# Performance work log

Measured on AMD Instinct MI355X. Metric: run time of the kernel, lower is better.

The kernel has to match this reference:

```python
import jax, jax.numpy as jnp
import numpy as np

N_ATOMS = 1_000_000
N_PAIRS = 32_000_000
N_MOL = 10_000

def setup_inputs() -> dict:
    key = jax.random.key(0)
    k1, k2, k3, k4, k5 = jax.random.split(key, 5)
    charges = jax.random.normal(k1, (N_ATOMS, 1), dtype=jnp.float32)
    # distances in [0.5, 2.5) to avoid divide-by-zero
    pair_dist = jax.random.uniform(k2, (N_PAIRS,), dtype=jnp.float32, minval=0.5, maxval=2.5)
    pair_first = jax.random.randint(k3, (N_PAIRS,), 0, N_ATOMS)
    pair_second = jax.random.randint(k4, (N_PAIRS,), 0, N_ATOMS)
    mol_index = jax.random.randint(k5, (N_ATOMS,), 0, N_MOL)
    return {
        "charges": charges,
        "pair_dist": pair_dist,
        "pair_first": pair_first,
        "pair_second": pair_second,
        "mol_index": mol_index,
        "n_molecules": N_MOL,
        "energy_conversion_factor": jnp.float32(14.399645),
    }

def reference(charges, pair_dist, pair_first, pair_second, mol_index, n_molecules, energy_conversion_factor):
    n_atoms = charges.shape[0]
    # gather charge of second atom in each pair, scale by 1/r  -> [n_pairs, 1]
    voltage_pairs = energy_conversion_factor * (charges[pair_second] / pair_dist[:, None])
    # scatter-add pair voltages onto first atom -> [n_atoms, 1]
    voltage_atom = jax.ops.segment_sum(voltage_pairs, pair_first, num_segments=n_atoms)
    # per-atom coulomb energy, then segment-sum over molecules
    coulomb_atom = voltage_atom * charges
    coulomb_molecules = 0.5 * jax.ops.segment_sum(coulomb_atom, mol_index, num_segments=n_molecules)
    return coulomb_molecules, voltage_atom
```

## Files before the change

kernel.cpp:

```cpp
#include <hip/hip_runtime.h>
#include <hip/hip_fp16.h>

#define BUCKET_BITS 12
#define BUCKET_SIZE 4096
#define NB 256
#define PPB 8192
#define BLK_A 256
#define MOL_BLOCKS 64


__global__ void init_cursors(int* __restrict__ cur, int nbuckets, int cap) {
    int b = blockIdx.x * blockDim.x + threadIdx.x;
    if (b < nbuckets) cur[b] = b * cap;
}

__global__ __launch_bounds__(BLK_A) void pair_scatter(
    const int4*   __restrict__ first4,
    const int4*   __restrict__ second4,
    const float4* __restrict__ dist4,
    const float*  __restrict__ charges,
    const float*  __restrict__ ecf_p,
    int* __restrict__ cur,
    unsigned* __restrict__ entries,
    int n_pairs4) {
    __shared__ unsigned stag[PPB];
    __shared__ int hist[NB];
    __shared__ int scanA[NB];
    __shared__ int lofs[NB + 1];
    __shared__ int gadj[NB];

    const int tid = threadIdx.x;
    hist[tid] = 0;
    __syncthreads();

    const int groups = PPB / 4;
    const int base4 = blockIdx.x * groups;

    #pragma unroll
    for (int it = 0; it < groups / BLK_A; ++it) {
        int g = base4 + it * BLK_A + tid;
        if (g < n_pairs4) {
            int4 f = first4[g];
            atomicAdd(&hist[f.x >> BUCKET_BITS], 1);
            atomicAdd(&hist[f.y >> BUCKET_BITS], 1);
            atomicAdd(&hist[f.z >> BUCKET_BITS], 1);
            atomicAdd(&hist[f.w >> BUCKET_BITS], 1);
        }
    }
    __syncthreads();

    scanA[tid] = hist[tid];
    __syncthreads();
    for (int off = 1; off < NB; off <<= 1) {
        int v = scanA[tid];
        if (tid >= off) v += scanA[tid - off];
        __syncthreads();
        scanA[tid] = v;
        __syncthreads();
    }
    if (tid == 0) lofs[0] = 0;
    lofs[tid + 1] = scanA[tid];
    __syncthreads();

    int cnt = hist[tid];
    if (cnt > 0) gadj[tid] = atomicAdd(&cur[tid], cnt) - lofs[tid];
    hist[tid] = lofs[tid];
    __syncthreads();

    const float ecf = *ecf_p;

    #pragma unroll
    for (int it = 0; it < groups / BLK_A; ++it) {
        int g = base4 + it * BLK_A + tid;
        if (g < n_pairs4) {
            int4   f = first4[g];
            int4   s = second4[g];
            float4 d = dist4[g];
            float v0 = ecf * charges[s.x] / d.x;
            float v1 = ecf * charges[s.y] / d.y;
            float v2 = ecf * charges[s.z] / d.z;
            float v3 = ecf * charges[s.w] / d.w;
            int p0 = atomicAdd(&hist[f.x >> BUCKET_BITS], 1);
            stag[p0] = ((unsigned)(f.x & (BUCKET_SIZE - 1)) << 16) |
                       (unsigned)__half_as_ushort(__float2half(v0));
            int p1 = atomicAdd(&hist[f.y >> BUCKET_BITS], 1);
            stag[p1] = ((unsigned)(f.y & (BUCKET_SIZE - 1)) << 16) |
                       (unsigned)__half_as_ushort(__float2half(v1));
            int p2 = atomicAdd(&hist[f.z >> BUCKET_BITS], 1);
            stag[p2] = ((unsigned)(f.z & (BUCKET_SIZE - 1)) << 16) |
                       (unsigned)__half_as_ushort(__float2half(v2));
            int p3 = atomicAdd(&hist[f.w >> BUCKET_BITS], 1);
            stag[p3] = ((unsigned)(f.w & (BUCKET_SIZE - 1)) << 16) |
                       (unsigned)__half_as_ushort(__float2half(v3));
        }
    }
    __syncthreads();

    const int tot = lofs[NB];
    for (int i = tid; i < tot; i += BLK_A) {
        unsigned e = stag[i];
        int lo = 0, hi = NB - 1;
        #pragma unroll
        for (int s = 0; s < 8; ++s) {
            int mid = (lo + hi + 1) >> 1;
            if (lofs[mid] <= i) lo = mid; else hi = mid - 1;
        }
        entries[gadj[lo] + i] = e;
    }
}

__global__ __launch_bounds__(1024) void bucket_reduce(
    const unsigned* __restrict__ entries,
    const int* __restrict__ cur,
    float* __restrict__ voltage,
    int cap, int n_atoms) {
    __shared__ float volt[BUCKET_SIZE];
    const int b = blockIdx.x;
    for (int i = threadIdx.x; i < BUCKET_SIZE; i += blockDim.x) volt[i] = 0.f;
    __syncthreads();
    const int start = b * cap;
    const int end = cur[b];
    const int cnt = end - start;
    const int cnt4 = cnt >> 2;
    const uint4* e4p = (const uint4*)(entries + start);
    for (int i = threadIdx.x; i < cnt4; i += blockDim.x) {
        uint4 e = e4p[i];
        atomicAdd(&volt[e.x >> 16], __half2float(__ushort_as_half((unsigned short)(e.x & 0xFFFFu))));
        atomicAdd(&volt[e.y >> 16], __half2float(__ushort_as_half((unsigned short)(e.y & 0xFFFFu))));
        atomicAdd(&volt[e.z >> 16], __half2float(__ushort_as_half((unsigned short)(e.z & 0xFFFFu))));
        atomicAdd(&volt[e.w >> 16], __half2float(__ushort_as_half((unsigned short)(e.w & 0xFFFFu))));
    }
    for (int i = (cnt4 << 2) + threadIdx.x; i < cnt; i += blockDim.x) {
        unsigned e = entries[start + i];
        atomicAdd(&volt[e >> 16], __half2float(__ushort_as_half((unsigned short)(e & 0xFFFFu))));
    }
    __syncthreads();
    const int abase = b << BUCKET_BITS;
    const int nat = min(BUCKET_SIZE, n_atoms - abase);
    for (int i = threadIdx.x; i < nat; i += blockDim.x)
        voltage[abase + i] = volt[i];
}

__global__ __launch_bounds__(1024) void mol_partial(
    const float* __restrict__ charges,
    const float* __restrict__ voltage,
    const int*  __restrict__ mol_index,
    float* __restrict__ partials,
    int n_mol, int n_atoms) {
    extern __shared__ float smem[];
    for (int i = threadIdx.x; i < n_mol; i += blockDim.x) smem[i] = 0.f;
    __syncthreads();
    const int n4 = n_atoms >> 2;
    const int gid = blockIdx.x * blockDim.x + threadIdx.x;
    const int stride = gridDim.x * blockDim.x;
    const float4* c4p = (const float4*)charges;
    const float4* v4p = (const float4*)voltage;
    const int4*   m4p = (const int4*)mol_index;
    for (int i = gid; i < n4; i += stride) {
        float4 c = c4p[i]; float4 v = v4p[i]; int4 m = m4p[i];
        atomicAdd(&smem[m.x], 0.5f * v.x * c.x);
        atomicAdd(&smem[m.y], 0.5f * v.y * c.y);
        atomicAdd(&smem[m.z], 0.5f * v.z * c.z);
        atomicAdd(&smem[m.w], 0.5f * v.w * c.w);
    }
    for (int i = (n4 << 2) + gid; i < n_atoms; i += stride)
        atomicAdd(&smem[mol_index[i]], 0.5f * voltage[i] * charges[i]);
    __syncthreads();
    float* dst = partials + (size_t)blockIdx.x * n_mol;
    for (int i = threadIdx.x; i < n_mol; i += blockDim.x)
        dst[i] = smem[i];
}

__global__ void mol_final(const float* __restrict__ partials,
                          float* __restrict__ mol_out,
                          int n_mol, int nparts) {
    int m = blockIdx.x * blockDim.x + threadIdx.x;
    if (m >= n_mol) return;
    float s = 0.f;
    for (int p = 0; p < nparts; ++p) s += partials[(size_t)p * n_mol + m];
    mol_out[m] = s;
}


__global__ void coulomb_pair_direct(const float* __restrict__ dist,
                                    const int*  __restrict__ first,
                                    const int*  __restrict__ second,
                                    const float* __restrict__ charges,
                                    const float* __restrict__ ecf_p,
                                    float* __restrict__ voltage,
                                    int n_pairs) {
    int p = blockIdx.x * blockDim.x + threadIdx.x;
    if (p >= n_pairs) return;
    float v = (*ecf_p) * charges[second[p]] / dist[p];
    atomicAdd(&voltage[first[p]], v);
}

__global__ void coulomb_atom_direct(const float* __restrict__ charges,
                                    const float* __restrict__ voltage,
                                    const int*  __restrict__ mol_index,
                                    float* __restrict__ mol_out,
                                    int n_atoms) {
    int a = blockIdx.x * blockDim.x + threadIdx.x;
    if (a >= n_atoms) return;
    atomicAdd(&mol_out[mol_index[a]], 0.5f * voltage[a] * charges[a]);
}

extern "C" void kernel_launch(void* const* d_in, const int* in_sizes, int n_in,
                              void* d_out, int out_size, void* d_ws, size_t ws_size,
                              hipStream_t stream) {
    const float* charges     = (const float*)d_in[0];
    const float* pair_dist   = (const float*)d_in[1];
    const int*   pair_first  = (const int*)d_in[2];
    const int*   pair_second = (const int*)d_in[3];
    const int*   mol_index   = (const int*)d_in[4];
    const float* ecf_p       = (const float*)d_in[6];

    const int n_atoms = in_sizes[0];
    const int n_pairs = in_sizes[1];
    const int n_mol   = out_size - n_atoms;

    float* mol_out = (float*)d_out;
    float* voltage = (float*)d_out + n_mol;

    const int nbuckets = (n_atoms + BUCKET_SIZE - 1) >> BUCKET_BITS;
    long long capll = (long long)n_pairs / (nbuckets > 0 ? nbuckets : 1);
    capll += capll / 16 + 4096;
    capll = (capll + 3) & ~3LL;
    long long tot_entries = capll * nbuckets;
    size_t entries_bytes = (size_t)tot_entries * sizeof(unsigned);
    size_t cur_off = (entries_bytes + 255) & ~(size_t)255;
    size_t mol_off = (cur_off + (size_t)nbuckets * sizeof(int) + 255) & ~(size_t)255;
    size_t need_base = cur_off + (size_t)nbuckets * sizeof(int);
    size_t need_mol  = mol_off + (size_t)MOL_BLOCKS * n_mol * sizeof(float);

    const bool mol_lds_ok = (size_t)n_mol * sizeof(float) <= 60 * 1024;
    const bool fast = (nbuckets >= 1) && (nbuckets <= NB) &&
                      (tot_entries < 0x7fffffffLL) &&
                      ((n_pairs & 3) == 0) &&
                      (need_base <= ws_size);
    const bool mol_hier = fast && mol_lds_ok && (need_mol <= ws_size);

    if (fast) {
        unsigned* entries = (unsigned*)d_ws;
        int* cur = (int*)((char*)d_ws + cur_off);
        const int cap = (int)capll;

        init_cursors<<<1, 256, 0, stream>>>(cur, nbuckets, cap);

        const int n_pairs4 = n_pairs >> 2;
        const int nblocks = (n_pairs + PPB - 1) / PPB;
        pair_scatter<<<nblocks, BLK_A, 0, stream>>>(
            (const int4*)pair_first, (const int4*)pair_second,
            (const float4*)pair_dist, charges, ecf_p, cur, entries, n_pairs4);

        bucket_reduce<<<nbuckets, 1024, 0, stream>>>(entries, cur, voltage,
                                                     cap, n_atoms);

        if (mol_hier) {
            float* partials = (float*)((char*)d_ws + mol_off);
            mol_partial<<<MOL_BLOCKS, 1024, n_mol * sizeof(float), stream>>>(
                charges, voltage, mol_index, partials, n_mol, n_atoms);
            mol_final<<<(n_mol + 255) / 256, 256, 0, stream>>>(
                partials, mol_out, n_mol, MOL_BLOCKS);
        } else {
            hipMemsetAsync(d_out, 0, (size_t)n_mol * sizeof(float), stream);
            coulomb_atom_direct<<<(n_atoms + 255) / 256, 256, 0, stream>>>(
                charges, voltage, mol_index, mol_out, n_atoms);
        }
    } else {
        hipMemsetAsync(d_out, 0, (size_t)out_size * sizeof(float), stream);
        coulomb_pair_direct<<<(n_pairs + 255) / 256, 256, 0, stream>>>(
            pair_dist, pair_first, pair_second, charges, ecf_p, voltage, n_pairs);
        coulomb_atom_direct<<<(n_atoms + 255) / 256, 256, 0, stream>>>(
            charges, voltage, mol_index, mol_out, n_atoms);
    }
}
```

Before: 809.4 us.

## Load pairs once into registers, warp-shuffle scan, split bucket reduce across blocks

pair_scatter now reads first/second/dist only once, computes the packed entries into registers before the histogram, and uses 512-thread blocks with a wavefront shuffle scan in place of the shared-memory Hillis-Steele scan. bucket_reduce is split into four blocks per bucket that each accumulate part of the entries and atomically add their partial results into a voltage array zeroed beforehand. This removes the second global read of pair_first and raises parallelism in the reduce stage. The cost is more registers per thread, an extra memset, and global atomics on the voltage output.

```diff
diff --git a/kernel.cpp b/kernel.cpp
--- a/kernel.cpp
+++ b/kernel.cpp
@@ -5,7 +5,10 @@
 #define BUCKET_SIZE 4096
 #define NB 256
 #define PPB 8192
-#define BLK_A 256
+#define BLK_A 512
+#define ITERS (PPB / 4 / BLK_A)
+#define RBLK 512
+#define RSPLIT 4
 #define MOL_BLOCKS 64
 
 
@@ -14,7 +17,7 @@
     if (b < nbuckets) cur[b] = b * cap;
 }
 
-__global__ __launch_bounds__(BLK_A) void pair_scatter(
+__global__ __launch_bounds__(BLK_A, 8) void pair_scatter(
     const int4*   __restrict__ first4,
     const int4*   __restrict__ second4,
     const float4* __restrict__ dist4,
@@ -25,73 +28,98 @@
     int n_pairs4) {
     __shared__ unsigned stag[PPB];
     __shared__ int hist[NB];
-    __shared__ int scanA[NB];
     __shared__ int lofs[NB + 1];
     __shared__ int gadj[NB];
+    __shared__ int wsum[NB / 64];
 
     const int tid = threadIdx.x;
-    hist[tid] = 0;
-    __syncthreads();
-
-    const int groups = PPB / 4;
-    const int base4 = blockIdx.x * groups;
-
+    const int base4 = blockIdx.x * (PPB / 4);
+    const float ecf = *ecf_p;
+
+    if (tid < NB) hist[tid] = 0;
+
+    int4 f4[ITERS];
+    unsigned ent[ITERS][4];
     #pragma unroll
-    for (int it = 0; it < groups / BLK_A; ++it) {
+    for (int it = 0; it < ITERS; ++it) {
         int g = base4 + it * BLK_A + tid;
         if (g < n_pairs4) {
-            int4 f = first4[g];
-            atomicAdd(&hist[f.x >> BUCKET_BITS], 1);
-            atomicAdd(&hist[f.y >> BUCKET_BITS], 1);
-            atomicAdd(&hist[f.z >> BUCKET_BITS], 1);
-            atomicAdd(&hist[f.w >> BUCKET_BITS], 1);
-        }
-    }
-    __syncthreads();
-
-    scanA[tid] = hist[tid];
-    __syncthreads();
-    for (int off = 1; off < NB; off <<= 1) {
-        int v = scanA[tid];
-        if (tid >= off) v += scanA[tid - off];
-        __syncthreads();
-        scanA[tid] = v;
-        __syncthreads();
-    }
-    if (tid == 0) lofs[0] = 0;
-    lofs[tid + 1] = scanA[tid];
-    __syncthreads();
-
-    int cnt = hist[tid];
-    if (cnt > 0) gadj[tid] = atomicAdd(&cur[tid], cnt) - lofs[tid];
-    hist[tid] = lofs[tid];
-    __syncthreads();
-
-    const float ecf = *ecf_p;
-
-    #pragma unroll
-    for (int it = 0; it < groups / BLK_A; ++it) {
-        int g = base4 + it * BLK_A + tid;
-        if (g < n_pairs4) {
-            int4   f = first4[g];
+            f4[it] = first4[g];
             int4   s = second4[g];
             float4 d = dist4[g];
-            float v0 = ecf * charges[s.x] / d.x;
-            float v1 = ecf * charges[s.y] / d.y;
-            float v2 = ecf * charges[s.z] / d.z;
-            float v3 = ecf * charges[s.w] / d.w;
-            int p0 = atomicAdd(&hist[f.x >> BUCKET_BITS], 1);
-            stag[p0] = ((unsigned)(f.x & (BUCKET_SIZE - 1)) << 16) |
-                       (unsigned)__half_as_ushort(__float2half(v0));
-            int p1 = atomicAdd(&hist[f.y >> BUCKET_BITS], 1);
-            stag[p1] = ((unsigned)(f.y & (BUCKET_SIZE - 1)) << 16) |
-                       (unsigned)__half_as_ushort(__float2half(v1));
-            int p2 = atomicAdd(&hist[f.z >> BUCKET_BITS], 1);
-            stag[p2] = ((unsigned)(f.z & (BUCKET_SIZE - 1)) << 16) |
-                       (unsigned)__half_as_ushort(__float2half(v2));
-            int p3 = atomicAdd(&hist[f.w >> BUCKET_BITS], 1);
-            stag[p3] = ((unsigned)(f.w & (BUCKET_SIZE - 1)) << 16) |
-                       (unsigned)__half_as_ushort(__float2half(v3));
+            float c0 = charges[s.x];
+            float c1 = charges[s.y];
+            float c2 = charges[s.z];
+            float c3 = charges[s.w];
+            float v0 = ecf * c0 / d.x;
+            float v1 = ecf * c1 / d.y;
+            float v2 = ecf * c2 / d.z;
+            float v3 = ecf * c3 / d.w;
+            ent[it][0] = ((unsigned)(f4[it].x & (BUCKET_SIZE - 1)) << 16) |
+                         (unsigned)__half_as_ushort(__float2half(v0));
+            ent[it][1] = ((unsigned)(f4[it].y & (BUCKET_SIZE - 1)) << 16) |
+                         (unsigned)__half_as_ushort(__float2half(v1));
+            ent[it][2] = ((unsigned)(f4[it].z & (BUCKET_SIZE - 1)) << 16) |
+                         (unsigned)__half_as_ushort(__float2half(v2));
+            ent[it][3] = ((unsigned)(f4[it].w & (BUCKET_SIZE - 1)) << 16) |
+                         (unsigned)__half_as_ushort(__float2half(v3));
+        } else {
+            f4[it] = make_int4(-1, -1, -1, -1);
+            ent[it][0] = ent[it][1] = ent[it][2] = ent[it][3] = 0u;
+        }
+    }
+    __syncthreads();
+
+    #pragma unroll
+    for (int it = 0; it < ITERS; ++it) {
+        if (f4[it].x >= 0) {
+            atomicAdd(&hist[f4[it].x >> BUCKET_BITS], 1);
+            atomicAdd(&hist[f4[it].y >> BUCKET_BITS], 1);
+            atomicAdd(&hist[f4[it].z >> BUCKET_BITS], 1);
+            atomicAdd(&hist[f4[it].w >> BUCKET_BITS], 1);
+        }
+    }
+    __syncthreads();
+
+    int cnt = 0, v = 0;
+    if (tid < NB) {
+        cnt = hist[tid];
+        v = cnt;
+        #pragma unroll
+        for (int off = 1; off < 64; off <<= 1) {
+            int n = __shfl_up(v, off);
+            if ((tid & 63) >= off) v += n;
+        }
+        if ((tid & 63) == 63) wsum[tid >> 6] = v;
+    }
+    __syncthreads();
+    if (tid == 0) {
+        int r = 0;
+        #pragma unroll
+        for (int w = 0; w < NB / 64; ++w) { int t = wsum[w]; wsum[w] = r; r += t; }
+    }
+    __syncthreads();
+    if (tid < NB) {
+        int incl = v + wsum[tid >> 6];
+        int excl = incl - cnt;
+        lofs[tid + 1] = incl;
+        if (tid == 0) lofs[0] = 0;
+        if (cnt > 0) gadj[tid] = atomicAdd(&cur[tid], cnt) - excl;
+        hist[tid] = excl;
+    }
+    __syncthreads();
+
+    #pragma unroll
+    for (int it = 0; it < ITERS; ++it) {
+        if (f4[it].x >= 0) {
+            int p0 = atomicAdd(&hist[f4[it].x >> BUCKET_BITS], 1);
+            stag[p0] = ent[it][0];
+            int p1 = atomicAdd(&hist[f4[it].y >> BUCKET_BITS], 1);
+            stag[p1] = ent[it][1];
+            int p2 = atomicAdd(&hist[f4[it].z >> BUCKET_BITS], 1);
+            stag[p2] = ent[it][2];
+            int p3 = atomicAdd(&hist[f4[it].w >> BUCKET_BITS], 1);
+            stag[p3] = ent[it][3];
         }
     }
     __syncthreads();
@@ -109,36 +137,41 @@
     }
 }
 
-__global__ __launch_bounds__(1024) void bucket_reduce(
+__global__ __launch_bounds__(RBLK) void bucket_reduce(
     const unsigned* __restrict__ entries,
     const int* __restrict__ cur,
     float* __restrict__ voltage,
     int cap, int n_atoms) {
     __shared__ float volt[BUCKET_SIZE];
-    const int b = blockIdx.x;
-    for (int i = threadIdx.x; i < BUCKET_SIZE; i += blockDim.x) volt[i] = 0.f;
+    const int b    = blockIdx.x / RSPLIT;
+    const int part = blockIdx.x % RSPLIT;
+    for (int i = threadIdx.x; i < BUCKET_SIZE; i += RBLK) volt[i] = 0.f;
     __syncthreads();
     const int start = b * cap;
-    const int end = cur[b];
-    const int cnt = end - start;
+    const int cnt = cur[b] - start;
     const int cnt4 = cnt >> 2;
+    const int chunk = (cnt4 + RSPLIT - 1) / RSPLIT;
+    const int lo = part * chunk;
+    const int hi = min(cnt4, lo + chunk);
     const uint4* e4p = (const uint4*)(entries + start);
-    for (int i = threadIdx.x; i < cnt4; i += blockDim.x) {
+    for (int i = lo + threadIdx.x; i < hi; i += RBLK) {
         uint4 e = e4p[i];
         atomicAdd(&volt[e.x >> 16], __half2float(__ushort_as_half((unsigned short)(e.x & 0xFFFFu))));
         atomicAdd(&volt[e.y >> 16], __half2float(__ushort_as_half((unsigned short)(e.y & 0xFFFFu))));
         atomicAdd(&volt[e.z >> 16], __half2float(__ushort_as_half((unsigned short)(e.z & 0xFFFFu))));
         atomicAdd(&volt[e.w >> 16], __half2float(__ushort_as_half((unsigned short)(e.w & 0xFFFFu))));
     }
-    for (int i = (cnt4 << 2) + threadIdx.x; i < cnt; i += blockDim.x) {
-        unsigned e = entries[start + i];
-        atomicAdd(&volt[e >> 16], __half2float(__ushort_as_half((unsigned short)(e & 0xFFFFu))));
+    if (part == RSPLIT - 1) {
+        for (int i = (cnt4 << 2) + threadIdx.x; i < cnt; i += RBLK) {
+            unsigned e = entries[start + i];
+            atomicAdd(&volt[e >> 16], __half2float(__ushort_as_half((unsigned short)(e & 0xFFFFu))));
+        }
     }
     __syncthreads();
     const int abase = b << BUCKET_BITS;
     const int nat = min(BUCKET_SIZE, n_atoms - abase);
-    for (int i = threadIdx.x; i < nat; i += blockDim.x)
-        voltage[abase + i] = volt[i];
+    for (int i = threadIdx.x; i < nat; i += RBLK)
+        atomicAdd(&voltage[abase + i], volt[i]);
 }
 
 __global__ __launch_bounds__(1024) void mol_partial(
@@ -247,14 +280,20 @@
 
         init_cursors<<<1, 256, 0, stream>>>(cur, nbuckets, cap);
 
+        if (mol_hier) {
+            hipMemsetAsync(voltage, 0, (size_t)n_atoms * sizeof(float), stream);
+        } else {
+            hipMemsetAsync(d_out, 0, (size_t)out_size * sizeof(float), stream);
+        }
+
         const int n_pairs4 = n_pairs >> 2;
         const int nblocks = (n_pairs + PPB - 1) / PPB;
         pair_scatter<<<nblocks, BLK_A, 0, stream>>>(
             (const int4*)pair_first, (const int4*)pair_second,
             (const float4*)pair_dist, charges, ecf_p, cur, entries, n_pairs4);
 
-        bucket_reduce<<<nbuckets, 1024, 0, stream>>>(entries, cur, voltage,
-                                                     cap, n_atoms);
+        bucket_reduce<<<nbuckets * RSPLIT, RBLK, 0, stream>>>(
+            entries, cur, voltage, cap, n_atoms);
 
         if (mol_hier) {
             float* partials = (float*)((char*)d_ws + mol_off);
@@ -263,7 +302,6 @@
             mol_final<<<(n_mol + 255) / 256, 256, 0, stream>>>(
                 partials, mol_out, n_mol, MOL_BLOCKS);
         } else {
-            hipMemsetAsync(d_out, 0, (size_t)n_mol * sizeof(float), stream);
             coulomb_atom_direct<<<(n_atoms + 255) / 256, 256, 0, stream>>>(
                 charges, voltage, mol_index, mol_out, n_atoms);
         }
```

New measurement: 782.5 us. 1.03x faster.
